# Kernel optimization log

Measured on AMD Instinct MI355X. Metric: run time of the kernel, lower is better.

## Reference

```python
import jax, jax.numpy as jnp
import numpy as np

QMIN, QMAX = -128.0, 127.0  # symmetric int8 (bit_width=8)

def setup_inputs() -> dict:
    key = jax.random.key(0)
    k1, k2, k3, k4, k5 = jax.random.split(key, 5)
    x = jax.random.normal(k1, (16, 4096, 1024), dtype=jnp.float32)
    weight_int = jax.random.randint(k2, (1024, 1024), 0, 127, dtype=jnp.int32)
    bias_int = jax.random.randint(k3, (1024,), 0, 127, dtype=jnp.int32)
    input_scale = jax.random.uniform(k4, (), dtype=jnp.float32, minval=0.01, maxval=1.0)
    output_scale = jax.random.uniform(k5, (), dtype=jnp.float32, minval=0.01, maxval=1.0)
    return {
        "x": x,
        "weight_int": weight_int,
        "bias_int": bias_int,
        "input_scale": input_scale,
        "output_scale": output_scale,
        "input_zero_point": 0,
        "output_zero_point": 0,
    }

def reference(x, weight_int, bias_int, input_scale, output_scale,
              input_zero_point, output_zero_point):
    # quantize input: round(x/scale)+zp, clamp to int8 range (kept in fp32,
    # matching x_int.float() in the original before the GEMM)
    x_q = jnp.clip(jnp.round(x / input_scale) + input_zero_point, QMIN, QMAX)
    # F.linear(x_q, W, b): [B,S,K] @ [N,K]^T + [N]
    out_int = jnp.einsum('bsk,nk->bsn', x_q, weight_int.astype(jnp.float32))
    out_int = out_int + bias_int.astype(jnp.float32)
    # dequantize output
    return (out_int - output_zero_point) * output_scale
```

## Files before the change

kernel.cpp:

```cpp
#include <hip/hip_runtime.h>
#include <stdint.h>

typedef int v4i __attribute__((ext_vector_type(4)));

#define AS1(p) ((const __attribute__((address_space(1))) void*)(p))
#define AS3(p) ((__attribute__((address_space(3))) void*)(p))

__global__ __launch_bounds__(256) void quant_x_kernel(
    const float* __restrict__ x, int8_t* __restrict__ xq,
    const float* __restrict__ s_p, const int* __restrict__ izp_p, int n16)
{
    int t = blockIdx.x * 256 + threadIdx.x;
    if (t >= n16) return;
    float s = *s_p;
    float zp = (float)(*izp_p);
    const float4* xin = (const float4*)x + (size_t)t * 4;
    int words[4];
#pragma unroll
    for (int i = 0; i < 4; ++i) {
        float4 v = xin[i];
        float q0 = fminf(127.f, fmaxf(-128.f, rintf(v.x / s) + zp));
        float q1 = fminf(127.f, fmaxf(-128.f, rintf(v.y / s) + zp));
        float q2 = fminf(127.f, fmaxf(-128.f, rintf(v.z / s) + zp));
        float q3 = fminf(127.f, fmaxf(-128.f, rintf(v.w / s) + zp));
        words[i] = ((int)q0 & 255) | (((int)q1 & 255) << 8) |
                   (((int)q2 & 255) << 16) | (((int)q3 & 255) << 24);
    }
    ((int4*)xq)[t] = make_int4(words[0], words[1], words[2], words[3]);
}

__global__ __launch_bounds__(256) void pack_w_kernel(
    const int* __restrict__ w, int8_t* __restrict__ w8, int n4)
{
    int t = blockIdx.x * 256 + threadIdx.x;
    if (t >= n4) return;
    int4 v = ((const int4*)w)[t];
    ((int*)w8)[t] = (v.x & 255) | ((v.y & 255) << 8) |
                    ((v.z & 255) << 16) | ((v.w & 255) << 24);
}

#define GM 65536
#define GN 1024
#define GK 1024
#define NT 16

__global__ __launch_bounds__(512) void gemm_i8_kernel(
    const int8_t* __restrict__ A,
    const int8_t* __restrict__ B,
    const int* __restrict__ bias,
    const float* __restrict__ osc_p, const int* __restrict__ ozp_p,
    float* __restrict__ out)
{
    __shared__ int8_t lds[4][2][16384];

    const int tid = threadIdx.x;
    const int w = tid >> 6, l = tid & 63;
    const int wm = w >> 2, wn = w & 3;
    const int r15 = l & 15, s4 = l >> 4;

    const int wg = blockIdx.x;
    const int lg = ((wg & 7) << 7) + (wg >> 3);
    const int bm0 = (lg >> 2) << 8;
    const int bn0 = (lg & 3) << 8;

    const int8_t* a_src[2];
    const int8_t* b_src[2];
    int st_dst[2];
#pragma unroll
    for (int e = 0; e < 2; ++e) {
        int o = ((w * 2 + e) << 10) + (l << 4);
        int row = o >> 6;
        int slot = (o >> 4) & 3;
        int gcol = ((slot ^ ((row >> 1) & 3)) << 4);
        a_src[e] = A + (size_t)(bm0 + row) * GK + gcol;
        b_src[e] = B + (size_t)(bn0 + row) * GK + gcol;
        st_dst[e] = (w * 2 + e) << 10;
    }

    int a_off[8], b_off[4];
#pragma unroll
    for (int i = 0; i < 8; ++i) {
        int row = wm * 128 + i * 16 + r15;
        a_off[i] = (row << 6) + ((s4 ^ ((row >> 1) & 3)) << 4);
    }
#pragma unroll
    for (int j = 0; j < 4; ++j) {
        int row = wn * 64 + j * 16 + r15;
        b_off[j] = (row << 6) + ((s4 ^ ((row >> 1) & 3)) << 4);
    }

    v4i acc[8][4];
#pragma unroll
    for (int i = 0; i < 8; ++i)
#pragma unroll
        for (int j = 0; j < 4; ++j) acc[i][j] = (v4i){0, 0, 0, 0};

#define STAGE(T, BUF) do { \
    __builtin_amdgcn_global_load_lds(AS1(a_src[0] + (T) * 64), AS3(&lds[BUF][0][st_dst[0]]), 16, 0, 0); \
    __builtin_amdgcn_global_load_lds(AS1(a_src[1] + (T) * 64), AS3(&lds[BUF][0][st_dst[1]]), 16, 0, 0); \
    __builtin_amdgcn_global_load_lds(AS1(b_src[0] + (T) * 64), AS3(&lds[BUF][1][st_dst[0]]), 16, 0, 0); \
    __builtin_amdgcn_global_load_lds(AS1(b_src[1] + (T) * 64), AS3(&lds[BUF][1][st_dst[1]]), 16, 0, 0); \
} while (0)

#define COMPUTE(BUF) do { \
    v4i af[8], bf[4]; \
    _Pragma("unroll") \
    for (int j = 0; j < 4; ++j) bf[j] = *(const v4i*)&lds[BUF][1][b_off[j]]; \
    _Pragma("unroll") \
    for (int i = 0; i < 8; ++i) af[i] = *(const v4i*)&lds[BUF][0][a_off[i]]; \
    __builtin_amdgcn_s_setprio(1); \
    _Pragma("unroll") \
    for (int i = 0; i < 8; ++i) \
    _Pragma("unroll") \
        for (int j = 0; j < 4; ++j) \
            acc[i][j] = __builtin_amdgcn_mfma_i32_16x16x64_i8(af[i], bf[j], acc[i][j], 0, 0, 0); \
    __builtin_amdgcn_s_setprio(0); \
} while (0)

    STAGE(0, 0); STAGE(1, 1); STAGE(2, 2);

#pragma unroll 1
    for (int t = 0; t < NT - 3; ++t) {
        asm volatile("s_waitcnt vmcnt(8)" ::: "memory");
        __builtin_amdgcn_s_barrier();
        STAGE(t + 3, (t + 3) & 3);
        COMPUTE(t & 3);
    }
    asm volatile("s_waitcnt vmcnt(8)" ::: "memory");
    __builtin_amdgcn_s_barrier();
    COMPUTE(1);
    asm volatile("s_waitcnt vmcnt(4)" ::: "memory");
    __builtin_amdgcn_s_barrier();
    COMPUTE(2);
    asm volatile("s_waitcnt vmcnt(0)" ::: "memory");
    __builtin_amdgcn_s_barrier();
    COMPUTE(3);

#undef STAGE
#undef COMPUTE

    const float osc = *osc_p;
    const int ozp = *ozp_p;
    int bj[4];
#pragma unroll
    for (int j = 0; j < 4; ++j)
        bj[j] = bias[bn0 + wn * 64 + j * 16 + r15] - ozp;

#pragma unroll
    for (int i = 0; i < 8; ++i) {
        const int mrow = bm0 + wm * 128 + i * 16 + s4 * 4;
#pragma unroll
        for (int j = 0; j < 4; ++j) {
            const int n = bn0 + wn * 64 + j * 16 + r15;
            float* op = out + (size_t)mrow * GN + n;
#pragma unroll
            for (int r = 0; r < 4; ++r)
                __builtin_nontemporal_store((float)(acc[i][j][r] + bj[j]) * osc,
                                            op + (size_t)r * GN);
        }
    }
}

extern "C" void kernel_launch(void* const* d_in, const int* in_sizes, int n_in,
                              void* d_out, int out_size, void* d_ws, size_t ws_size,
                              hipStream_t stream)
{
    const float* x         = (const float*)d_in[0];
    const int*   w_int     = (const int*)d_in[1];
    const int*   b_int     = (const int*)d_in[2];
    const float* in_scale  = (const float*)d_in[3];
    const float* out_scale = (const float*)d_in[4];
    const int*   izp       = (const int*)d_in[5];
    const int*   ozp       = (const int*)d_in[6];
    float* out = (float*)d_out;

    int8_t* xq = (int8_t*)d_ws;
    int8_t* w8 = (int8_t*)d_ws + (size_t)64 * 1024 * 1024;

    quant_x_kernel<<<16384, 256, 0, stream>>>(x, xq, in_scale, izp, 4194304);
    pack_w_kernel<<<1024, 256, 0, stream>>>(w_int, w8, 262144);
    gemm_i8_kernel<<<1024, 512, 0, stream>>>(xq, w8, b_int, out_scale, ozp, out);
}
```

Baseline: 164.6 us.

## Fuse input quantization into the int8 GEMM with full-N row tiles

Removes the separate quantize kernel and the int8 intermediate buffer for x. The GEMM now loads fp32 x tiles into LDS, quantizes them in-kernel, and computes 32-row by full-1024-column output tiles, with each block streaming all of B through a double-buffered LDS stage. This cuts the HBM round trip of the quantized activations and the launch, but every block rereads the whole weight matrix. A-tile reuse per B load is also low, and the large LDS footprint may limit occupancy.

```diff
diff --git a/kernel.cpp b/kernel.cpp
--- a/kernel.cpp
+++ b/kernel.cpp
@@ -5,29 +5,6 @@
 
 #define AS1(p) ((const __attribute__((address_space(1))) void*)(p))
 #define AS3(p) ((__attribute__((address_space(3))) void*)(p))
-
-__global__ __launch_bounds__(256) void quant_x_kernel(
-    const float* __restrict__ x, int8_t* __restrict__ xq,
-    const float* __restrict__ s_p, const int* __restrict__ izp_p, int n16)
-{
-    int t = blockIdx.x * 256 + threadIdx.x;
-    if (t >= n16) return;
-    float s = *s_p;
-    float zp = (float)(*izp_p);
-    const float4* xin = (const float4*)x + (size_t)t * 4;
-    int words[4];
-#pragma unroll
-    for (int i = 0; i < 4; ++i) {
-        float4 v = xin[i];
-        float q0 = fminf(127.f, fmaxf(-128.f, rintf(v.x / s) + zp));
-        float q1 = fminf(127.f, fmaxf(-128.f, rintf(v.y / s) + zp));
-        float q2 = fminf(127.f, fmaxf(-128.f, rintf(v.z / s) + zp));
-        float q3 = fminf(127.f, fmaxf(-128.f, rintf(v.w / s) + zp));
-        words[i] = ((int)q0 & 255) | (((int)q1 & 255) << 8) |
-                   (((int)q2 & 255) << 16) | (((int)q3 & 255) << 24);
-    }
-    ((int4*)xq)[t] = make_int4(words[0], words[1], words[2], words[3]);
-}
 
 __global__ __launch_bounds__(256) void pack_w_kernel(
     const int* __restrict__ w, int8_t* __restrict__ w8, int n4)
@@ -44,114 +21,141 @@
 #define GK 1024
 #define NT 16
 
-__global__ __launch_bounds__(512) void gemm_i8_kernel(
-    const int8_t* __restrict__ A,
-    const int8_t* __restrict__ B,
+__global__ __launch_bounds__(512, 2) void fused_kernel(
+    const float* __restrict__ X,
+    const int8_t* __restrict__ B8,
     const int* __restrict__ bias,
+    const float* __restrict__ isc_p, const int* __restrict__ izp_p,
     const float* __restrict__ osc_p, const int* __restrict__ ozp_p,
     float* __restrict__ out)
 {
-    __shared__ int8_t lds[4][2][16384];
+    __shared__ int8_t Bsb[2][65536];
+    __shared__ float  A32[2][2048];
+    __shared__ int8_t Asb[2][2048];
 
     const int tid = threadIdx.x;
-    const int w = tid >> 6, l = tid & 63;
-    const int wm = w >> 2, wn = w & 3;
-    const int r15 = l & 15, s4 = l >> 4;
+    const int w   = tid >> 6, l = tid & 63;
+    const int r15 = l & 15,  s4 = l >> 4;
+    const int bm0 = blockIdx.x << 5;
 
-    const int wg = blockIdx.x;
-    const int lg = ((wg & 7) << 7) + (wg >> 3);
-    const int bm0 = (lg >> 2) << 8;
-    const int bn0 = (lg & 3) << 8;
+    float isc_r = *isc_p;
+    float izp_r = (float)(*izp_p);
+    float isc, izp;
+    asm volatile("v_mov_b32 %0, %1" : "=v"(isc) : "v"(isc_r));
+    asm volatile("v_mov_b32 %0, %1" : "=v"(izp) : "v"(izp_r));
+    asm volatile("s_waitcnt vmcnt(0) lgkmcnt(0)" ::: "memory");
 
-    const int8_t* a_src[2];
-    const int8_t* b_src[2];
-    int st_dst[2];
+    const int8_t* b_base = B8 + (size_t)(w * 128 + (l >> 2)) * GK
+                              + ((((l & 3) ^ ((l >> 3) & 3))) << 4);
+
+    const float* a32_src = X + (size_t)(bm0 + w * 4 + (l >> 4)) * GK + ((l & 15) << 2);
+
+    const int a_dst = ((tid >> 4) << 6)
+                    + ((((tid >> 2) & 3) ^ ((tid >> 5) & 3)) << 4)
+                    + ((tid & 3) << 2);
+
+    int a_off[2], b_off[8];
 #pragma unroll
-    for (int e = 0; e < 2; ++e) {
-        int o = ((w * 2 + e) << 10) + (l << 4);
-        int row = o >> 6;
-        int slot = (o >> 4) & 3;
-        int gcol = ((slot ^ ((row >> 1) & 3)) << 4);
-        a_src[e] = A + (size_t)(bm0 + row) * GK + gcol;
-        b_src[e] = B + (size_t)(bn0 + row) * GK + gcol;
-        st_dst[e] = (w * 2 + e) << 10;
-    }
+    for (int i = 0; i < 2; ++i)
+        a_off[i] = ((i * 16 + r15) << 6) + ((s4 ^ ((r15 >> 1) & 3)) << 4);
+#pragma unroll
+    for (int j = 0; j < 8; ++j)
+        b_off[j] = ((w * 128 + j * 16 + r15) << 6) + ((s4 ^ ((r15 >> 1) & 3)) << 4);
 
-    int a_off[8], b_off[4];
+    v4i acc[2][8];
 #pragma unroll
-    for (int i = 0; i < 8; ++i) {
-        int row = wm * 128 + i * 16 + r15;
-        a_off[i] = (row << 6) + ((s4 ^ ((row >> 1) & 3)) << 4);
-    }
+    for (int i = 0; i < 2; ++i)
 #pragma unroll
-    for (int j = 0; j < 4; ++j) {
-        int row = wn * 64 + j * 16 + r15;
-        b_off[j] = (row << 6) + ((s4 ^ ((row >> 1) & 3)) << 4);
-    }
+        for (int j = 0; j < 8; ++j) acc[i][j] = (v4i){0, 0, 0, 0};
 
-    v4i acc[8][4];
-#pragma unroll
-    for (int i = 0; i < 8; ++i)
-#pragma unroll
-        for (int j = 0; j < 4; ++j) acc[i][j] = (v4i){0, 0, 0, 0};
+#define STAGE_B(T, BUF) do { \
+    _Pragma("unroll") \
+    for (int c = 0; c < 8; ++c) \
+        __builtin_amdgcn_global_load_lds( \
+            AS1(b_base + ((size_t)(c) << 14) + (T) * 64), \
+            AS3(&Bsb[BUF][(w * 8 + c) << 10]), 16, 0, 0); \
+} while (0)
 
-#define STAGE(T, BUF) do { \
-    __builtin_amdgcn_global_load_lds(AS1(a_src[0] + (T) * 64), AS3(&lds[BUF][0][st_dst[0]]), 16, 0, 0); \
-    __builtin_amdgcn_global_load_lds(AS1(a_src[1] + (T) * 64), AS3(&lds[BUF][0][st_dst[1]]), 16, 0, 0); \
-    __builtin_amdgcn_global_load_lds(AS1(b_src[0] + (T) * 64), AS3(&lds[BUF][1][st_dst[0]]), 16, 0, 0); \
-    __builtin_amdgcn_global_load_lds(AS1(b_src[1] + (T) * 64), AS3(&lds[BUF][1][st_dst[1]]), 16, 0, 0); \
+#define STAGE_A(T, BUF) \
+    __builtin_amdgcn_global_load_lds(AS1(a32_src + (T) * 64), \
+                                     AS3(&A32[BUF][w << 8]), 16, 0, 0)
+
+#define QUANT(BUF) do { \
+    float4 v_ = *(const float4*)&A32[BUF][tid << 2]; \
+    float q0 = fminf(127.f, fmaxf(-128.f, rintf(v_.x / isc) + izp)); \
+    float q1 = fminf(127.f, fmaxf(-128.f, rintf(v_.y / isc) + izp)); \
+    float q2 = fminf(127.f, fmaxf(-128.f, rintf(v_.z / isc) + izp)); \
+    float q3 = fminf(127.f, fmaxf(-128.f, rintf(v_.w / isc) + izp)); \
+    int wd_ = ((int)q0 & 255) | (((int)q1 & 255) << 8) | \
+              (((int)q2 & 255) << 16) | (((int)q3 & 255) << 24); \
+    *(int*)&Asb[BUF][a_dst] = wd_; \
 } while (0)
 
 #define COMPUTE(BUF) do { \
-    v4i af[8], bf[4]; \
-    _Pragma("unroll") \
-    for (int j = 0; j < 4; ++j) bf[j] = *(const v4i*)&lds[BUF][1][b_off[j]]; \
-    _Pragma("unroll") \
-    for (int i = 0; i < 8; ++i) af[i] = *(const v4i*)&lds[BUF][0][a_off[i]]; \
+    v4i af0 = *(const v4i*)&Asb[BUF][a_off[0]]; \
+    v4i af1 = *(const v4i*)&Asb[BUF][a_off[1]]; \
     __builtin_amdgcn_s_setprio(1); \
     _Pragma("unroll") \
-    for (int i = 0; i < 8; ++i) \
-    _Pragma("unroll") \
-        for (int j = 0; j < 4; ++j) \
-            acc[i][j] = __builtin_amdgcn_mfma_i32_16x16x64_i8(af[i], bf[j], acc[i][j], 0, 0, 0); \
+    for (int j = 0; j < 8; ++j) { \
+        v4i bf = *(const v4i*)&Bsb[BUF][b_off[j]]; \
+        acc[0][j] = __builtin_amdgcn_mfma_i32_16x16x64_i8(af0, bf, acc[0][j], 0, 0, 0); \
+        acc[1][j] = __builtin_amdgcn_mfma_i32_16x16x64_i8(af1, bf, acc[1][j], 0, 0, 0); \
+    } \
     __builtin_amdgcn_s_setprio(0); \
 } while (0)
 
-    STAGE(0, 0); STAGE(1, 1); STAGE(2, 2);
+#define BAR() do { \
+    asm volatile("s_waitcnt lgkmcnt(0)" ::: "memory"); \
+    __builtin_amdgcn_s_barrier(); \
+    __builtin_amdgcn_sched_barrier(0); \
+} while (0)
+
+    STAGE_A(0, 0);
+    STAGE_B(0, 0);
+    STAGE_A(1, 1);
+    asm volatile("s_waitcnt vmcnt(9)" ::: "memory");
+    QUANT(0);
+    asm volatile("s_waitcnt vmcnt(1)" ::: "memory");
+    BAR();
 
 #pragma unroll 1
-    for (int t = 0; t < NT - 3; ++t) {
-        asm volatile("s_waitcnt vmcnt(8)" ::: "memory");
-        __builtin_amdgcn_s_barrier();
-        STAGE(t + 3, (t + 3) & 3);
-        COMPUTE(t & 3);
+    for (int t = 0; t < NT - 2; ++t) {
+        STAGE_B(t + 1, (t + 1) & 1);
+        STAGE_A(t + 2, t & 1);
+        COMPUTE(t & 1);
+        asm volatile("s_waitcnt vmcnt(9)" ::: "memory");
+        QUANT((t + 1) & 1);
+        asm volatile("s_waitcnt vmcnt(1)" ::: "memory");
+        BAR();
     }
+
+    STAGE_B(15, 1);
+    COMPUTE(0);
     asm volatile("s_waitcnt vmcnt(8)" ::: "memory");
-    __builtin_amdgcn_s_barrier();
+    QUANT(1);
+    asm volatile("s_waitcnt vmcnt(0)" ::: "memory");
+    BAR();
     COMPUTE(1);
-    asm volatile("s_waitcnt vmcnt(4)" ::: "memory");
-    __builtin_amdgcn_s_barrier();
-    COMPUTE(2);
-    asm volatile("s_waitcnt vmcnt(0)" ::: "memory");
-    __builtin_amdgcn_s_barrier();
-    COMPUTE(3);
 
-#undef STAGE
+#undef STAGE_B
+#undef STAGE_A
+#undef QUANT
 #undef COMPUTE
+#undef BAR
 
     const float osc = *osc_p;
-    const int ozp = *ozp_p;
-    int bj[4];
+    const int   ozp = *ozp_p;
+    int bj[8];
 #pragma unroll
-    for (int j = 0; j < 4; ++j)
-        bj[j] = bias[bn0 + wn * 64 + j * 16 + r15] - ozp;
+    for (int j = 0; j < 8; ++j)
+        bj[j] = bias[w * 128 + j * 16 + r15] - ozp;
 
 #pragma unroll
-    for (int i = 0; i < 8; ++i) {
-        const int mrow = bm0 + wm * 128 + i * 16 + s4 * 4;
+    for (int i = 0; i < 2; ++i) {
+        const int mrow = bm0 + i * 16 + s4 * 4;
 #pragma unroll
-        for (int j = 0; j < 4; ++j) {
-            const int n = bn0 + wn * 64 + j * 16 + r15;
+        for (int j = 0; j < 8; ++j) {
+            const int n = w * 128 + j * 16 + r15;
             float* op = out + (size_t)mrow * GN + n;
 #pragma unroll
             for (int r = 0; r < 4; ++r)
@@ -174,10 +178,9 @@
     const int*   ozp       = (const int*)d_in[6];
     float* out = (float*)d_out;
 
-    int8_t* xq = (int8_t*)d_ws;
-    int8_t* w8 = (int8_t*)d_ws + (size_t)64 * 1024 * 1024;
+    int8_t* w8 = (int8_t*)d_ws;
 
-    quant_x_kernel<<<16384, 256, 0, stream>>>(x, xq, in_scale, izp, 4194304);
     pack_w_kernel<<<1024, 256, 0, stream>>>(w_int, w8, 262144);
-    gemm_i8_kernel<<<1024, 512, 0, stream>>>(xq, w8, b_int, out_scale, ozp, out);
+    fused_kernel<<<2048, 512, 0, stream>>>(x, w8, b_int,
+                                           in_scale, izp, out_scale, ozp, out);
 }
```

Result: slower. 287.2 us (+74.5%).

## Shrink GEMM tile to 128x128 with 4 waves and triple-buffered LDS

Applied to the files above, without the earlier changes.

Replaces the 256x256 block tile (8 waves, 4-stage LDS ring of 128KB) with a 128x128 tile computed by 4 waves, using a 3-stage rotating LDS buffer of 48KB and launching four times as many workgroups. The intent is higher occupancy (launch bounds requesting 3 blocks per CU), less LDS pressure and better load balance across CUs. In exchange, each block reuses its loaded data less, so more global/L2 traffic is needed per FLOP, and the prefetch depth drops from three tiles to two.

```diff
diff --git a/kernel.cpp b/kernel.cpp
--- a/kernel.cpp
+++ b/kernel.cpp
@@ -44,54 +44,54 @@
 #define GK 1024
 #define NT 16
 
-__global__ __launch_bounds__(512) void gemm_i8_kernel(
+__global__ __launch_bounds__(256, 3) void gemm_i8_kernel(
     const int8_t* __restrict__ A,
     const int8_t* __restrict__ B,
     const int* __restrict__ bias,
     const float* __restrict__ osc_p, const int* __restrict__ ozp_p,
     float* __restrict__ out)
 {
-    __shared__ int8_t lds[4][2][16384];
+    __shared__ int8_t lds[3][2][8192];
 
     const int tid = threadIdx.x;
     const int w = tid >> 6, l = tid & 63;
-    const int wm = w >> 2, wn = w & 3;
+    const int wr = w >> 1, wc = w & 1;
     const int r15 = l & 15, s4 = l >> 4;
 
     const int wg = blockIdx.x;
-    const int lg = ((wg & 7) << 7) + (wg >> 3);
-    const int bm0 = (lg >> 2) << 8;
-    const int bn0 = (lg & 3) << 8;
+    const int lg = ((wg & 7) << 9) + (wg >> 3);
+    const int bm0 = (lg >> 3) << 7;
+    const int bn0 = (lg & 7) << 7;
 
     const int8_t* a_src[2];
     const int8_t* b_src[2];
     int st_dst[2];
 #pragma unroll
     for (int e = 0; e < 2; ++e) {
-        int o = ((w * 2 + e) << 10) + (l << 4);
+        int o = e * 4096 + tid * 16;
         int row = o >> 6;
         int slot = (o >> 4) & 3;
         int gcol = ((slot ^ ((row >> 1) & 3)) << 4);
         a_src[e] = A + (size_t)(bm0 + row) * GK + gcol;
         b_src[e] = B + (size_t)(bn0 + row) * GK + gcol;
-        st_dst[e] = (w * 2 + e) << 10;
+        st_dst[e] = e * 4096 + w * 1024;
     }
 
-    int a_off[8], b_off[4];
+    int a_off[4], b_off[4];
 #pragma unroll
-    for (int i = 0; i < 8; ++i) {
-        int row = wm * 128 + i * 16 + r15;
+    for (int i = 0; i < 4; ++i) {
+        int row = wr * 64 + i * 16 + r15;
         a_off[i] = (row << 6) + ((s4 ^ ((row >> 1) & 3)) << 4);
     }
 #pragma unroll
     for (int j = 0; j < 4; ++j) {
-        int row = wn * 64 + j * 16 + r15;
+        int row = wc * 64 + j * 16 + r15;
         b_off[j] = (row << 6) + ((s4 ^ ((row >> 1) & 3)) << 4);
     }
 
-    v4i acc[8][4];
+    v4i acc[4][4];
 #pragma unroll
-    for (int i = 0; i < 8; ++i)
+    for (int i = 0; i < 4; ++i)
 #pragma unroll
         for (int j = 0; j < 4; ++j) acc[i][j] = (v4i){0, 0, 0, 0};
 
@@ -103,38 +103,38 @@
 } while (0)
 
 #define COMPUTE(BUF) do { \
-    v4i af[8], bf[4]; \
+    v4i af[4], bf[4]; \
     _Pragma("unroll") \
     for (int j = 0; j < 4; ++j) bf[j] = *(const v4i*)&lds[BUF][1][b_off[j]]; \
     _Pragma("unroll") \
-    for (int i = 0; i < 8; ++i) af[i] = *(const v4i*)&lds[BUF][0][a_off[i]]; \
+    for (int i = 0; i < 4; ++i) af[i] = *(const v4i*)&lds[BUF][0][a_off[i]]; \
     __builtin_amdgcn_s_setprio(1); \
     _Pragma("unroll") \
-    for (int i = 0; i < 8; ++i) \
+    for (int i = 0; i < 4; ++i) \
     _Pragma("unroll") \
         for (int j = 0; j < 4; ++j) \
             acc[i][j] = __builtin_amdgcn_mfma_i32_16x16x64_i8(af[i], bf[j], acc[i][j], 0, 0, 0); \
     __builtin_amdgcn_s_setprio(0); \
 } while (0)
 
-    STAGE(0, 0); STAGE(1, 1); STAGE(2, 2);
+    STAGE(0, 0);
+    STAGE(1, 1);
 
+    int c0 = 0, c1 = 1, c2 = 2;
 #pragma unroll 1
-    for (int t = 0; t < NT - 3; ++t) {
-        asm volatile("s_waitcnt vmcnt(8)" ::: "memory");
+    for (int t = 0; t < NT - 2; ++t) {
+        asm volatile("s_waitcnt vmcnt(4)" ::: "memory");
         __builtin_amdgcn_s_barrier();
-        STAGE(t + 3, (t + 3) & 3);
-        COMPUTE(t & 3);
+        STAGE(t + 2, c2);
+        COMPUTE(c0);
+        int tmp = c0; c0 = c1; c1 = c2; c2 = tmp;
     }
-    asm volatile("s_waitcnt vmcnt(8)" ::: "memory");
-    __builtin_amdgcn_s_barrier();
-    COMPUTE(1);
     asm volatile("s_waitcnt vmcnt(4)" ::: "memory");
     __builtin_amdgcn_s_barrier();
-    COMPUTE(2);
+    COMPUTE(c0);
     asm volatile("s_waitcnt vmcnt(0)" ::: "memory");
     __builtin_amdgcn_s_barrier();
-    COMPUTE(3);
+    COMPUTE(c1);
 
 #undef STAGE
 #undef COMPUTE
@@ -144,14 +144,14 @@
     int bj[4];
 #pragma unroll
     for (int j = 0; j < 4; ++j)
-        bj[j] = bias[bn0 + wn * 64 + j * 16 + r15] - ozp;
+        bj[j] = bias[bn0 + wc * 64 + j * 16 + r15] - ozp;
 
 #pragma unroll
-    for (int i = 0; i < 8; ++i) {
-        const int mrow = bm0 + wm * 128 + i * 16 + s4 * 4;
+    for (int i = 0; i < 4; ++i) {
+        const int mrow = bm0 + wr * 64 + i * 16 + s4 * 4;
 #pragma unroll
         for (int j = 0; j < 4; ++j) {
-            const int n = bn0 + wn * 64 + j * 16 + r15;
+            const int n = bn0 + wc * 64 + j * 16 + r15;
             float* op = out + (size_t)mrow * GN + n;
 #pragma unroll
             for (int r = 0; r < 4; ++r)
@@ -179,5 +179,5 @@
 
     quant_x_kernel<<<16384, 256, 0, stream>>>(x, xq, in_scale, izp, 4194304);
     pack_w_kernel<<<1024, 256, 0, stream>>>(w_int, w8, 262144);
-    gemm_i8_kernel<<<1024, 512, 0, stream>>>(xq, w8, b_int, out_scale, ozp, out);
+    gemm_i8_kernel<<<4096, 256, 0, stream>>>(xq, w8, b_int, out_scale, ozp, out);
 }
```

New measurement: 156.7 us. 1.05x faster.

## Restructure int8 GEMM to BK=128 double buffering with phased interleaved loads

Applied to the files above, without the earlier changes.

Raises the K tile from 64 to 128 bytes so there are 8 iterations instead of 16. The 4-deep LDS ring is replaced by a double buffer with an 8-way XOR swizzle. Each iteration is split into four phases, and each phase spreads the next tile's global-to-LDS loads between MFMA bursts separated by barriers. Launch bounds now ask for 2 blocks per CU, which caps registers per thread. The goal is fewer barriers per unit of work and better overlap of memory with MFMA. The cost is more barriers inside each iteration, a shallower prefetch, and possible register spills under the tighter occupancy bound.

```diff
diff --git a/kernel.cpp b/kernel.cpp
--- a/kernel.cpp
+++ b/kernel.cpp
@@ -42,52 +42,45 @@
 #define GM 65536
 #define GN 1024
 #define GK 1024
-#define NT 16
+#define NT 8
 
-__global__ __launch_bounds__(512) void gemm_i8_kernel(
+__global__ __launch_bounds__(512, 2) void gemm_i8_kernel(
     const int8_t* __restrict__ A,
     const int8_t* __restrict__ B,
     const int* __restrict__ bias,
     const float* __restrict__ osc_p, const int* __restrict__ ozp_p,
     float* __restrict__ out)
 {
-    __shared__ int8_t lds[4][2][16384];
+    __shared__ int8_t As[2][32768];
+    __shared__ int8_t Bs[2][32768];
 
     const int tid = threadIdx.x;
-    const int w = tid >> 6, l = tid & 63;
-    const int wm = w >> 2, wn = w & 3;
-    const int r15 = l & 15, s4 = l >> 4;
+    const int w   = tid >> 6, l = tid & 63;
+    const int wm  = w >> 2,  wn = w & 3;
+    const int r15 = l & 15,  s4 = l >> 4;
 
     const int wg = blockIdx.x;
     const int lg = ((wg & 7) << 7) + (wg >> 3);
     const int bm0 = (lg >> 2) << 8;
     const int bn0 = (lg & 3) << 8;
 
-    const int8_t* a_src[2];
-    const int8_t* b_src[2];
-    int st_dst[2];
-#pragma unroll
-    for (int e = 0; e < 2; ++e) {
-        int o = ((w * 2 + e) << 10) + (l << 4);
-        int row = o >> 6;
-        int slot = (o >> 4) & 3;
-        int gcol = ((slot ^ ((row >> 1) & 3)) << 4);
-        a_src[e] = A + (size_t)(bm0 + row) * GK + gcol;
-        b_src[e] = B + (size_t)(bn0 + row) * GK + gcol;
-        st_dst[e] = (w * 2 + e) << 10;
-    }
+    const int srow = tid >> 3;
+    const int gcol = (((tid & 7) ^ ((tid >> 3) & 7)) << 4);
+    const int8_t* aS = A + (size_t)(bm0 + srow) * GK + gcol;
+    const int8_t* bS = B + (size_t)(bn0 + srow) * GK + gcol;
 
-    int a_off[8], b_off[4];
-#pragma unroll
-    for (int i = 0; i < 8; ++i) {
-        int row = wm * 128 + i * 16 + r15;
-        a_off[i] = (row << 6) + ((s4 ^ ((row >> 1) & 3)) << 4);
-    }
-#pragma unroll
-    for (int j = 0; j < 4; ++j) {
-        int row = wn * 64 + j * 16 + r15;
-        b_off[j] = (row << 6) + ((s4 ^ ((row >> 1) & 3)) << 4);
-    }
+#define SHOT_A(T, BUF, C) __builtin_amdgcn_global_load_lds( \
+    AS1(aS + (size_t)(C) * 64 * GK + (T) * 128), \
+    AS3(&As[BUF][(C) * 8192 + w * 1024]), 16, 0, 0)
+#define SHOT_B(T, BUF, C) __builtin_amdgcn_global_load_lds( \
+    AS1(bS + (size_t)(C) * 64 * GK + (T) * 128), \
+    AS3(&Bs[BUF][(C) * 8192 + w * 1024]), 16, 0, 0)
+
+    const int akey = r15 & 7;
+    const int a_rd0 = ((wm * 128 + r15) << 7) + (((0 + s4) ^ akey) << 4);
+    const int a_rd1 = ((wm * 128 + r15) << 7) + (((4 + s4) ^ akey) << 4);
+    const int b_rd0 = ((wn * 64 + r15) << 7) + (((0 + s4) ^ akey) << 4);
+    const int b_rd1 = ((wn * 64 + r15) << 7) + (((4 + s4) ^ akey) << 4);
 
     v4i acc[8][4];
 #pragma unroll
@@ -95,52 +88,67 @@
 #pragma unroll
         for (int j = 0; j < 4; ++j) acc[i][j] = (v4i){0, 0, 0, 0};
 
-#define STAGE(T, BUF) do { \
-    __builtin_amdgcn_global_load_lds(AS1(a_src[0] + (T) * 64), AS3(&lds[BUF][0][st_dst[0]]), 16, 0, 0); \
-    __builtin_amdgcn_global_load_lds(AS1(a_src[1] + (T) * 64), AS3(&lds[BUF][0][st_dst[1]]), 16, 0, 0); \
-    __builtin_amdgcn_global_load_lds(AS1(b_src[0] + (T) * 64), AS3(&lds[BUF][1][st_dst[0]]), 16, 0, 0); \
-    __builtin_amdgcn_global_load_lds(AS1(b_src[1] + (T) * 64), AS3(&lds[BUF][1][st_dst[1]]), 16, 0, 0); \
+    v4i bfr[4][2];
+
+#define LOADB(CUR) do { \
+    _Pragma("unroll") \
+    for (int j = 0; j < 4; ++j) { \
+        bfr[j][0] = *(const v4i*)&Bs[CUR][b_rd0 + j * 2048]; \
+        bfr[j][1] = *(const v4i*)&Bs[CUR][b_rd1 + j * 2048]; \
+    } \
 } while (0)
 
-#define COMPUTE(BUF) do { \
-    v4i af[8], bf[4]; \
-    _Pragma("unroll") \
-    for (int j = 0; j < 4; ++j) bf[j] = *(const v4i*)&lds[BUF][1][b_off[j]]; \
-    _Pragma("unroll") \
-    for (int i = 0; i < 8; ++i) af[i] = *(const v4i*)&lds[BUF][0][a_off[i]]; \
+#define PHASE(CUR, Q, ...) do { \
+    v4i af0 = *(const v4i*)&As[CUR][a_rd0 + (Q) * 4096]; \
+    v4i af1 = *(const v4i*)&As[CUR][a_rd1 + (Q) * 4096]; \
+    v4i af2 = *(const v4i*)&As[CUR][a_rd0 + (Q) * 4096 + 2048]; \
+    v4i af3 = *(const v4i*)&As[CUR][a_rd1 + (Q) * 4096 + 2048]; \
+    __VA_ARGS__; \
+    __builtin_amdgcn_s_barrier(); \
     __builtin_amdgcn_s_setprio(1); \
     _Pragma("unroll") \
-    for (int i = 0; i < 8; ++i) \
-    _Pragma("unroll") \
-        for (int j = 0; j < 4; ++j) \
-            acc[i][j] = __builtin_amdgcn_mfma_i32_16x16x64_i8(af[i], bf[j], acc[i][j], 0, 0, 0); \
+    for (int j = 0; j < 4; ++j) { \
+        acc[(Q)*2][j]     = __builtin_amdgcn_mfma_i32_16x16x64_i8(af0, bfr[j][0], acc[(Q)*2][j], 0, 0, 0); \
+        acc[(Q)*2][j]     = __builtin_amdgcn_mfma_i32_16x16x64_i8(af1, bfr[j][1], acc[(Q)*2][j], 0, 0, 0); \
+        acc[(Q)*2 + 1][j] = __builtin_amdgcn_mfma_i32_16x16x64_i8(af2, bfr[j][0], acc[(Q)*2 + 1][j], 0, 0, 0); \
+        acc[(Q)*2 + 1][j] = __builtin_amdgcn_mfma_i32_16x16x64_i8(af3, bfr[j][1], acc[(Q)*2 + 1][j], 0, 0, 0); \
+    } \
     __builtin_amdgcn_s_setprio(0); \
+    __builtin_amdgcn_s_barrier(); \
 } while (0)
 
-    STAGE(0, 0); STAGE(1, 1); STAGE(2, 2);
+#define BODY(T, SON) do { \
+    const int cur_ = (T) & 1, nxt_ = cur_ ^ 1; \
+    if (SON) { \
+        SHOT_A((T) + 1, nxt_, 0); SHOT_A((T) + 1, nxt_, 1); \
+        asm volatile("s_waitcnt vmcnt(2)" ::: "memory"); \
+    } else { \
+        asm volatile("s_waitcnt vmcnt(0)" ::: "memory"); \
+    } \
+    __builtin_amdgcn_s_barrier(); \
+    __builtin_amdgcn_sched_barrier(0); \
+    LOADB(cur_); \
+    PHASE(cur_, 0, if (SON) { SHOT_A((T) + 1, nxt_, 2); SHOT_A((T) + 1, nxt_, 3); }); \
+    PHASE(cur_, 1, if (SON) { SHOT_B((T) + 1, nxt_, 0); SHOT_B((T) + 1, nxt_, 1); }); \
+    PHASE(cur_, 2, if (SON) { SHOT_B((T) + 1, nxt_, 2); SHOT_B((T) + 1, nxt_, 3); }); \
+    PHASE(cur_, 3, ); \
+} while (0)
+
+#pragma unroll
+    for (int c = 0; c < 4; ++c) { SHOT_A(0, 0, c); SHOT_B(0, 0, c); }
 
 #pragma unroll 1
-    for (int t = 0; t < NT - 3; ++t) {
-        asm volatile("s_waitcnt vmcnt(8)" ::: "memory");
-        __builtin_amdgcn_s_barrier();
-        STAGE(t + 3, (t + 3) & 3);
-        COMPUTE(t & 3);
-    }
-    asm volatile("s_waitcnt vmcnt(8)" ::: "memory");
-    __builtin_amdgcn_s_barrier();
-    COMPUTE(1);
-    asm volatile("s_waitcnt vmcnt(4)" ::: "memory");
-    __builtin_amdgcn_s_barrier();
-    COMPUTE(2);
-    asm volatile("s_waitcnt vmcnt(0)" ::: "memory");
-    __builtin_amdgcn_s_barrier();
-    COMPUTE(3);
+    for (int t = 0; t < NT - 1; ++t) BODY(t, 1);
+    BODY(NT - 1, 0);
 
-#undef STAGE
-#undef COMPUTE
+#undef BODY
+#undef PHASE
+#undef LOADB
+#undef SHOT_A
+#undef SHOT_B
 
     const float osc = *osc_p;
-    const int ozp = *ozp_p;
+    const int   ozp = *ozp_p;
     int bj[4];
 #pragma unroll
     for (int j = 0; j < 4; ++j)
```

Result: slower. 171.3 us (+4.1%).
